# Optimization experiments

Hardware: AMD Instinct MI355X
Metric: run time of the kernel (lower is better)

Reference implementation:

```python
import jax, jax.numpy as jnp
import numpy as np

B, S, D_IN, D_OUT, DEPTH = 4, 2048, 2048, 2048, 11
N_NODES = 2 ** (DEPTH + 1) - 1  # 4095


def setup_inputs() -> dict:
    key = jax.random.key(0)
    k1, k2, k3 = jax.random.split(key, 3)
    x = jax.random.normal(k1, (B, S, D_IN), dtype=jnp.float32)
    # scale weights like Linear init (~1/sqrt(fan_in)) to keep logits sane
    w_in = jax.random.normal(k2, (N_NODES, D_IN), dtype=jnp.float32) * (1.0 / np.sqrt(D_IN))
    w_out = jax.random.normal(k3, (D_OUT, N_NODES), dtype=jnp.float32) * (1.0 / np.sqrt(N_NODES))
    return {"x": x, "w_in": w_in, "w_out": w_out}


def reference(x, w_in, w_out):
    # x: [B,S,D_in]; w_in: [n_nodes, D_in]; w_out: [D_out, n_nodes]
    b, s, _ = x.shape
    cur = jnp.zeros((b, s), dtype=jnp.int32)
    nodes, logits = [], []
    for _ in range(DEPTH + 1):  # fixed, small depth loop (12 iters)
        nodes.append(cur)
        coeffs = w_in[cur]                       # [B,S,D_in] data-dependent gather
        score = jnp.einsum('bsd,bsd->bs', x, coeffs)  # per-token dot product
        logits.append(score)
        cur = cur * 2 + (score >= 0).astype(jnp.int32) + 1
    all_nodes = jnp.stack(nodes, axis=-1)        # [B,S,depth+1]
    all_logits = jnp.stack(logits, axis=-1)      # [B,S,depth+1]
    sel = w_out.T[all_nodes]                     # [B,S,depth+1,D_out]
    mlp1 = jax.nn.gelu(all_logits, approximate=False)  # torch nn.GELU default = exact erf
    return jnp.einsum('bsl,bslw->bsw', mlp1, sel)      # [B,S,D_out]
```

## Files before the change

kernel.cpp:

```cpp
#include <hip/hip_runtime.h>


#define D_IN    2048
#define D_OUT   2048
#define DEPTHP1 12
#define N_NODES 4095
#define N_TOK   8192
#define N_LEAF  2048

__global__ __launch_bounds__(256) void transpose_wout64(
    const float* __restrict__ in, float* __restrict__ out) {
    __shared__ float tile[64][65];
    const int n0 = blockIdx.x * 64;
    const int j0 = blockIdx.y * 64;
    const int tx = threadIdx.x;
    const int ty = threadIdx.y;
    const int n = n0 + tx;
#pragma unroll
    for (int k = 0; k < 16; k++) {
        const int r = ty * 16 + k;
        if (n < N_NODES) tile[r][tx] = in[(size_t)(j0 + r) * N_NODES + n];
    }
    __syncthreads();
#pragma unroll
    for (int k = 0; k < 16; k++) {
        const int r = ty * 16 + k;
        const int nn = n0 + r;
        if (nn < N_NODES) out[(size_t)nn * D_OUT + (j0 + tx)] = tile[tx][r];
    }
}

__global__ __launch_bounds__(256) void phaseA(
    const float* __restrict__ x,
    const float* __restrict__ w_in,
    float* __restrict__ g_all,
    int* __restrict__ leaf,
    int* __restrict__ hist) {
    extern __shared__ float xs[];
    const int wave  = threadIdx.x >> 6;
    const int lane  = threadIdx.x & 63;
    const int token = blockIdx.x * 4 + wave;

    float4* xw = (float4*)(xs) + wave * (D_IN / 4);
    const float4* xrow = (const float4*)(x + (size_t)token * D_IN);
#pragma unroll
    for (int c = 0; c < 8; c++) xw[lane + 64 * c] = xrow[lane + 64 * c];

    int cur = 0;
#pragma unroll
    for (int l = 0; l < DEPTHP1; l++) {
        const float4* wrow = (const float4*)(w_in + (size_t)cur * D_IN);
        float p0 = 0.f, p1 = 0.f, p2 = 0.f, p3 = 0.f;
#pragma unroll
        for (int c = 0; c < 8; c++) {
            const float4 wc = wrow[lane + 64 * c];
            const float4 xc = xw[lane + 64 * c];
            float* p = (c < 2) ? &p0 : (c < 4) ? &p1 : (c < 6) ? &p2 : &p3;
            *p += wc.x * xc.x + wc.y * xc.y + wc.z * xc.z + wc.w * xc.w;
        }
        float part = (p0 + p1) + (p2 + p3);
#pragma unroll
        for (int off = 32; off >= 1; off >>= 1)
            part += __shfl_xor(part, off, 64);
        const float score = part;
        cur = 2 * cur + 1 + (score >= 0.f ? 1 : 0);
        const float g = 0.5f * score * (1.0f + erff(score * 0.70710678118654752f));
        if (lane == 0) g_all[token * DEPTHP1 + l] = g;
    }
    if (lane == 0) {
        const int leafid = ((cur - 1) >> 1) - (N_LEAF - 1);
        leaf[token] = leafid;
        atomicAdd(&hist[leafid], 1);
    }
}

__global__ __launch_bounds__(256) void init_counts(int* __restrict__ p) {
    const int i = blockIdx.x * 256 + threadIdx.x;
    if (i < 2 * N_LEAF) p[i] = 0;
}

__global__ __launch_bounds__(256) void scan2048(
    const int* __restrict__ hist, int* __restrict__ offsets ) {
    __shared__ int vals[N_LEAF];
    __shared__ int partial[256];
    const int t = threadIdx.x;
    int sum = 0;
#pragma unroll
    for (int k = 0; k < 8; k++) {
        const int v = hist[t * 8 + k];
        vals[t * 8 + k] = v;
        sum += v;
    }
    partial[t] = sum;
    __syncthreads();
    for (int off = 1; off < 256; off <<= 1) {
        const int v  = partial[t];
        const int vo = (t >= off) ? partial[t - off] : 0;
        __syncthreads();
        partial[t] = v + vo;
        __syncthreads();
    }
    int base = (t > 0) ? partial[t - 1] : 0;
#pragma unroll
    for (int k = 0; k < 8; k++) {
        offsets[t * 8 + k] = base;
        base += vals[t * 8 + k];
    }
    if (t == 255) offsets[N_LEAF] = base;
}

__global__ __launch_bounds__(256) void scatter_tokens(
    const int* __restrict__ leaf, const int* __restrict__ offsets,
    int* __restrict__ cnt, const float* __restrict__ g_all,
    int* __restrict__ order, float* __restrict__ g_sorted) {
    const int t = blockIdx.x * 256 + threadIdx.x;
    if (t < N_TOK) {
        const int lf = leaf[t];
        const int pos = offsets[lf] + atomicAdd(&cnt[lf], 1);
        order[pos] = t;
#pragma unroll
        for (int l = 0; l < DEPTHP1; l++)
            g_sorted[(size_t)pos * DEPTHP1 + l] = g_all[(size_t)t * DEPTHP1 + l];
    }
}

__global__ __launch_bounds__(256, 2) void phaseB(
    const float* __restrict__ w_out_t,
    const float* __restrict__ g_sorted,
    const int* __restrict__ order,
    const int* __restrict__ offsets,
    float* __restrict__ out) {
    const int lf = ((blockIdx.x & 7) << 8) | (blockIdx.x >> 3);
    const int start = offsets[lf];
    const int end   = offsets[lf + 1];
    if (start == end) return;
    const int t = threadIdx.x;

    int nodes[DEPTHP1];
    const int L = lf + N_LEAF;
#pragma unroll
    for (int l = 0; l < DEPTHP1; l++) nodes[l] = (L >> (DEPTHP1 - 1 - l)) - 1;

    for (int cs = start; cs < end; cs += 8) {
        const int T = end - cs;
        float acc[8][8];
#pragma unroll
        for (int tt = 0; tt < 8; tt++)
#pragma unroll
            for (int k = 0; k < 8; k++) acc[tt][k] = 0.f;

#pragma unroll
        for (int l = 0; l < DEPTHP1; l++) {
            const float4* wr = (const float4*)(w_out_t + (size_t)nodes[l] * D_OUT);
            const float4 w0 = wr[t * 2 + 0];
            const float4 w1 = wr[t * 2 + 1];
#pragma unroll
            for (int tt = 0; tt < 8; tt++) {
                const float g = (tt < T)
                    ? g_sorted[(size_t)(cs + tt) * DEPTHP1 + l] : 0.f;
                acc[tt][0] += g * w0.x; acc[tt][1] += g * w0.y;
                acc[tt][2] += g * w0.z; acc[tt][3] += g * w0.w;
                acc[tt][4] += g * w1.x; acc[tt][5] += g * w1.y;
                acc[tt][6] += g * w1.z; acc[tt][7] += g * w1.w;
            }
        }
#pragma unroll
        for (int tt = 0; tt < 8; tt++) {
            if (tt < T) {
                const int tok = order[cs + tt];
                float4* po = (float4*)(out + (size_t)tok * D_OUT + t * 8);
                float4 o0, o1;
                o0.x = acc[tt][0]; o0.y = acc[tt][1];
                o0.z = acc[tt][2]; o0.w = acc[tt][3];
                o1.x = acc[tt][4]; o1.y = acc[tt][5];
                o1.z = acc[tt][6]; o1.w = acc[tt][7];
                po[0] = o0; po[1] = o1;
            }
        }
    }
}

template <bool TRANSPOSED>
__global__ __launch_bounds__(256) void fff_fused(
    const float* __restrict__ x, const float* __restrict__ w_in,
    const float* __restrict__ w_out, float* __restrict__ out) {
    const int wave  = threadIdx.x >> 6;
    const int lane  = threadIdx.x & 63;
    const int token = blockIdx.x * 4 + wave;
    const float4* xrow = (const float4*)(x + (size_t)token * D_IN);
    float xf[32];
#pragma unroll
    for (int c = 0; c < 8; c++) {
        float4 xc = xrow[lane + 64 * c];
        xf[c * 4 + 0] = xc.x; xf[c * 4 + 1] = xc.y;
        xf[c * 4 + 2] = xc.z; xf[c * 4 + 3] = xc.w;
    }
    float acc[32];
#pragma unroll
    for (int k = 0; k < 32; k++) acc[k] = 0.f;
    int cur = 0;
#pragma unroll
    for (int l = 0; l < DEPTHP1; l++) {
        const float4* wrow = (const float4*)(w_in + (size_t)cur * D_IN);
        float part = 0.f;
#pragma unroll
        for (int c = 0; c < 8; c++) {
            float4 wc = wrow[lane + 64 * c];
            part += wc.x * xf[c * 4 + 0]; part += wc.y * xf[c * 4 + 1];
            part += wc.z * xf[c * 4 + 2]; part += wc.w * xf[c * 4 + 3];
        }
#pragma unroll
        for (int off = 32; off >= 1; off >>= 1) part += __shfl_xor(part, off, 64);
        const float score = part;
        const float g = 0.5f * score * (1.0f + erff(score * 0.70710678118654752f));
        if (TRANSPOSED) {
            const float4* orow = (const float4*)(w_out + (size_t)cur * D_OUT);
#pragma unroll
            for (int c = 0; c < 8; c++) {
                float4 oc = orow[lane + 64 * c];
                acc[c * 4 + 0] += g * oc.x; acc[c * 4 + 1] += g * oc.y;
                acc[c * 4 + 2] += g * oc.z; acc[c * 4 + 3] += g * oc.w;
            }
        } else {
#pragma unroll
            for (int c = 0; c < 8; c++)
#pragma unroll
                for (int k = 0; k < 4; k++) {
                    const int j = (lane + 64 * c) * 4 + k;
                    acc[c * 4 + k] += g * w_out[(size_t)j * N_NODES + cur];
                }
        }
        cur = 2 * cur + 1 + (score >= 0.f ? 1 : 0);
    }
    float4* outrow = (float4*)(out + (size_t)token * D_OUT);
#pragma unroll
    for (int c = 0; c < 8; c++) {
        float4 o;
        o.x = acc[c * 4 + 0]; o.y = acc[c * 4 + 1];
        o.z = acc[c * 4 + 2]; o.w = acc[c * 4 + 3];
        outrow[lane + 64 * c] = o;
    }
}

extern "C" void kernel_launch(void* const* d_in, const int* in_sizes, int n_in,
                              void* d_out, int out_size, void* d_ws, size_t ws_size,
                              hipStream_t stream) {
    (void)in_sizes; (void)n_in; (void)out_size;
    const float* x     = (const float*)d_in[0];
    const float* w_in  = (const float*)d_in[1];
    const float* w_out = (const float*)d_in[2];
    float* out = (float*)d_out;

    const size_t wt_bytes   = (size_t)N_NODES * D_OUT * sizeof(float);
    const size_t g_bytes    = (size_t)N_TOK * DEPTHP1 * sizeof(float);
    const size_t leaf_bytes = (size_t)N_TOK * sizeof(int);
    const size_t ord_bytes  = (size_t)N_TOK * sizeof(int);
    const size_t hist_bytes = (size_t)N_LEAF * sizeof(int);
    const size_t cnt_bytes  = (size_t)N_LEAF * sizeof(int);
    const size_t offs_bytes = (size_t)(N_LEAF + 1) * sizeof(int);
    const size_t gs_bytes   = g_bytes;
    const size_t need = wt_bytes + g_bytes + leaf_bytes + ord_bytes +
                        hist_bytes + cnt_bytes + offs_bytes + gs_bytes + 64;

    if (ws_size >= need) {
        char* p = (char*)d_ws;
        float* w_out_t  = (float*)p;  p += wt_bytes;
        float* g_all    = (float*)p;  p += g_bytes;
        int*   leaf     = (int*)p;    p += leaf_bytes;
        int*   order    = (int*)p;    p += ord_bytes;
        int*   hist     = (int*)p;    p += hist_bytes;
        int*   cnt      = (int*)p;    p += cnt_bytes;
        int*   offsets  = (int*)p;    p += offs_bytes;
        float* g_sorted = (float*)p;

        init_counts<<<(2 * N_LEAF + 255) / 256, 256, 0, stream>>>(hist);
        transpose_wout64<<<dim3((N_NODES + 63) / 64, D_OUT / 64), dim3(64, 4),
                           0, stream>>>(w_out, w_out_t);
        phaseA<<<N_TOK / 4, 256, 4 * D_IN * sizeof(float), stream>>>(
            x, w_in, g_all, leaf, hist);
        scan2048<<<1, 256, 0, stream>>>(hist, offsets);
        scatter_tokens<<<N_TOK / 256, 256, 0, stream>>>(leaf, offsets, cnt,
                                                        g_all, order, g_sorted);
        phaseB<<<N_LEAF, 256, 0, stream>>>(w_out_t, g_sorted, order, offsets, out);
    } else if (ws_size >= wt_bytes) {
        float* w_out_t = (float*)d_ws;
        transpose_wout64<<<dim3((N_NODES + 63) / 64, D_OUT / 64), dim3(64, 4),
                           0, stream>>>(w_out, w_out_t);
        fff_fused<true><<<N_TOK / 4, 256, 0, stream>>>(x, w_in, w_out_t, out);
    } else {
        fff_fused<false><<<N_TOK / 4, 256, 0, stream>>>(x, w_in, w_out, out);
    }
}
```

Baseline: 232.2 us.

## Fuse transpose into routing kernel and replace sort pipeline with per-leaf token scan

Merges the w_out transpose and the tree-routing pass into one launch by interleaving blocks, so the transpose runs alongside routing. The histogram, scan and scatter kernels are removed. Instead, each leaf block of the output phase scans all 8192 leaf ids and collects its own tokens into shared memory with an LDS atomic. This cuts the pipeline from six launches to two and drops the global atomics and sorted copies. In exchange, every one of the 2048 blocks rereads the full leaf array, uses 32KB of LDS, and the token order within a leaf is no longer deterministic.

```diff
diff --git a/kernel.cpp b/kernel.cpp
--- a/kernel.cpp
+++ b/kernel.cpp
@@ -7,6 +7,138 @@
 #define N_NODES 4095
 #define N_TOK   8192
 #define N_LEAF  2048
+
+__global__ __launch_bounds__(256, 4) void fusedA(
+    const float* __restrict__ x,
+    const float* __restrict__ w_in,
+    const float* __restrict__ w_out,
+    float* __restrict__ w_out_t,
+    float* __restrict__ g_all,
+    int* __restrict__ leaf) {
+    extern __shared__ char smem[];
+
+    if (blockIdx.x & 1) {
+        float (*tile)[65] = (float(*)[65])smem;
+        const int tb = blockIdx.x >> 1;
+        const int n0 = (tb & 63) * 64;
+        const int j0 = (tb >> 6) * 64;
+        const int tx = threadIdx.x & 63;
+        const int ty = threadIdx.x >> 6;
+        const int n = n0 + tx;
+#pragma unroll
+        for (int k = 0; k < 16; k++) {
+            const int r = ty * 16 + k;
+            if (n < N_NODES) tile[r][tx] = w_out[(size_t)(j0 + r) * N_NODES + n];
+        }
+        __syncthreads();
+#pragma unroll
+        for (int k = 0; k < 16; k++) {
+            const int r = ty * 16 + k;
+            const int nn = n0 + r;
+            if (nn < N_NODES) w_out_t[(size_t)nn * D_OUT + (j0 + tx)] = tile[tx][r];
+        }
+        return;
+    }
+
+    float* xs = (float*)smem;
+    const int wave  = threadIdx.x >> 6;
+    const int lane  = threadIdx.x & 63;
+    const int token = (blockIdx.x >> 1) * 4 + wave;
+
+    float4* xw = (float4*)xs + wave * (D_IN / 4);
+    const float4* xrow = (const float4*)(x + (size_t)token * D_IN);
+#pragma unroll
+    for (int c = 0; c < 8; c++) xw[lane + 64 * c] = xrow[lane + 64 * c];
+
+    int cur = 0;
+#pragma unroll
+    for (int l = 0; l < DEPTHP1; l++) {
+        const float4* wrow = (const float4*)(w_in + (size_t)cur * D_IN);
+        float4 wv[8];
+#pragma unroll
+        for (int c = 0; c < 8; c++) wv[c] = wrow[lane + 64 * c];
+        float p0 = 0.f, p1 = 0.f, p2 = 0.f, p3 = 0.f;
+#pragma unroll
+        for (int c = 0; c < 8; c++) {
+            const float4 xc = xw[lane + 64 * c];
+            float* p = (c < 2) ? &p0 : (c < 4) ? &p1 : (c < 6) ? &p2 : &p3;
+            *p += wv[c].x * xc.x + wv[c].y * xc.y + wv[c].z * xc.z + wv[c].w * xc.w;
+        }
+        float part = (p0 + p1) + (p2 + p3);
+#pragma unroll
+        for (int off = 32; off >= 1; off >>= 1)
+            part += __shfl_xor(part, off, 64);
+        const float score = part;
+        cur = 2 * cur + 1 + (score >= 0.f ? 1 : 0);
+        const float g = 0.5f * score * (1.0f + erff(score * 0.70710678118654752f));
+        if (lane == 0) g_all[token * DEPTHP1 + l] = g;
+    }
+    if (lane == 0) leaf[token] = ((cur - 1) >> 1) - (N_LEAF - 1);
+}
+
+__global__ __launch_bounds__(256, 2) void phaseB2(
+    const float* __restrict__ w_out_t,
+    const float* __restrict__ g_all,
+    const int* __restrict__ leaf,
+    float* __restrict__ out) {
+    const int lf = ((blockIdx.x & 7) << 8) | (blockIdx.x >> 3);
+    __shared__ int toks[N_TOK];
+    __shared__ int lcount;
+    const int t = threadIdx.x;
+    if (t == 0) lcount = 0;
+    __syncthreads();
+#pragma unroll
+    for (int k = 0; k < N_TOK / 256; k++) {
+        const int tok = k * 256 + t;
+        if (leaf[tok] == lf) toks[atomicAdd(&lcount, 1)] = tok;
+    }
+    __syncthreads();
+    const int n = lcount;
+    if (n == 0) return;
+
+    int nodes[DEPTHP1];
+    const int L = lf + N_LEAF;
+#pragma unroll
+    for (int l = 0; l < DEPTHP1; l++) nodes[l] = (L >> (DEPTHP1 - 1 - l)) - 1;
+
+    for (int cs = 0; cs < n; cs += 8) {
+        const int T = n - cs;
+        float acc[8][8];
+#pragma unroll
+        for (int tt = 0; tt < 8; tt++)
+#pragma unroll
+            for (int k = 0; k < 8; k++) acc[tt][k] = 0.f;
+
+#pragma unroll
+        for (int l = 0; l < DEPTHP1; l++) {
+            const float4* wr = (const float4*)(w_out_t + (size_t)nodes[l] * D_OUT);
+            const float4 w0 = wr[t * 2 + 0];
+            const float4 w1 = wr[t * 2 + 1];
+#pragma unroll
+            for (int tt = 0; tt < 8; tt++) {
+                const float g = (tt < T)
+                    ? g_all[(size_t)toks[cs + tt] * DEPTHP1 + l] : 0.f;
+                acc[tt][0] += g * w0.x; acc[tt][1] += g * w0.y;
+                acc[tt][2] += g * w0.z; acc[tt][3] += g * w0.w;
+                acc[tt][4] += g * w1.x; acc[tt][5] += g * w1.y;
+                acc[tt][6] += g * w1.z; acc[tt][7] += g * w1.w;
+            }
+        }
+#pragma unroll
+        for (int tt = 0; tt < 8; tt++) {
+            if (tt < T) {
+                const int tok = toks[cs + tt];
+                float4* po = (float4*)(out + (size_t)tok * D_OUT + t * 8);
+                float4 o0, o1;
+                o0.x = acc[tt][0]; o0.y = acc[tt][1];
+                o0.z = acc[tt][2]; o0.w = acc[tt][3];
+                o1.x = acc[tt][4]; o1.y = acc[tt][5];
+                o1.z = acc[tt][6]; o1.w = acc[tt][7];
+                po[0] = o0; po[1] = o1;
+            }
+        }
+    }
+}
 
 __global__ __launch_bounds__(256) void transpose_wout64(
     const float* __restrict__ in, float* __restrict__ out) {
@@ -27,156 +159,6 @@
         const int r = ty * 16 + k;
         const int nn = n0 + r;
         if (nn < N_NODES) out[(size_t)nn * D_OUT + (j0 + tx)] = tile[tx][r];
-    }
-}
-
-__global__ __launch_bounds__(256) void phaseA(
-    const float* __restrict__ x,
-    const float* __restrict__ w_in,
-    float* __restrict__ g_all,
-    int* __restrict__ leaf,
-    int* __restrict__ hist) {
-    extern __shared__ float xs[];
-    const int wave  = threadIdx.x >> 6;
-    const int lane  = threadIdx.x & 63;
-    const int token = blockIdx.x * 4 + wave;
-
-    float4* xw = (float4*)(xs) + wave * (D_IN / 4);
-    const float4* xrow = (const float4*)(x + (size_t)token * D_IN);
-#pragma unroll
-    for (int c = 0; c < 8; c++) xw[lane + 64 * c] = xrow[lane + 64 * c];
-
-    int cur = 0;
-#pragma unroll
-    for (int l = 0; l < DEPTHP1; l++) {
-        const float4* wrow = (const float4*)(w_in + (size_t)cur * D_IN);
-        float p0 = 0.f, p1 = 0.f, p2 = 0.f, p3 = 0.f;
-#pragma unroll
-        for (int c = 0; c < 8; c++) {
-            const float4 wc = wrow[lane + 64 * c];
-            const float4 xc = xw[lane + 64 * c];
-            float* p = (c < 2) ? &p0 : (c < 4) ? &p1 : (c < 6) ? &p2 : &p3;
-            *p += wc.x * xc.x + wc.y * xc.y + wc.z * xc.z + wc.w * xc.w;
-        }
-        float part = (p0 + p1) + (p2 + p3);
-#pragma unroll
-        for (int off = 32; off >= 1; off >>= 1)
-            part += __shfl_xor(part, off, 64);
-        const float score = part;
-        cur = 2 * cur + 1 + (score >= 0.f ? 1 : 0);
-        const float g = 0.5f * score * (1.0f + erff(score * 0.70710678118654752f));
-        if (lane == 0) g_all[token * DEPTHP1 + l] = g;
-    }
-    if (lane == 0) {
-        const int leafid = ((cur - 1) >> 1) - (N_LEAF - 1);
-        leaf[token] = leafid;
-        atomicAdd(&hist[leafid], 1);
-    }
-}
-
-__global__ __launch_bounds__(256) void init_counts(int* __restrict__ p) {
-    const int i = blockIdx.x * 256 + threadIdx.x;
-    if (i < 2 * N_LEAF) p[i] = 0;
-}
-
-__global__ __launch_bounds__(256) void scan2048(
-    const int* __restrict__ hist, int* __restrict__ offsets ) {
-    __shared__ int vals[N_LEAF];
-    __shared__ int partial[256];
-    const int t = threadIdx.x;
-    int sum = 0;
-#pragma unroll
-    for (int k = 0; k < 8; k++) {
-        const int v = hist[t * 8 + k];
-        vals[t * 8 + k] = v;
-        sum += v;
-    }
-    partial[t] = sum;
-    __syncthreads();
-    for (int off = 1; off < 256; off <<= 1) {
-        const int v  = partial[t];
-        const int vo = (t >= off) ? partial[t - off] : 0;
-        __syncthreads();
-        partial[t] = v + vo;
-        __syncthreads();
-    }
-    int base = (t > 0) ? partial[t - 1] : 0;
-#pragma unroll
-    for (int k = 0; k < 8; k++) {
-        offsets[t * 8 + k] = base;
-        base += vals[t * 8 + k];
-    }
-    if (t == 255) offsets[N_LEAF] = base;
-}
-
-__global__ __launch_bounds__(256) void scatter_tokens(
-    const int* __restrict__ leaf, const int* __restrict__ offsets,
-    int* __restrict__ cnt, const float* __restrict__ g_all,
-    int* __restrict__ order, float* __restrict__ g_sorted) {
-    const int t = blockIdx.x * 256 + threadIdx.x;
-    if (t < N_TOK) {
-        const int lf = leaf[t];
-        const int pos = offsets[lf] + atomicAdd(&cnt[lf], 1);
-        order[pos] = t;
-#pragma unroll
-        for (int l = 0; l < DEPTHP1; l++)
-            g_sorted[(size_t)pos * DEPTHP1 + l] = g_all[(size_t)t * DEPTHP1 + l];
-    }
-}
-
-__global__ __launch_bounds__(256, 2) void phaseB(
-    const float* __restrict__ w_out_t,
-    const float* __restrict__ g_sorted,
-    const int* __restrict__ order,
-    const int* __restrict__ offsets,
-    float* __restrict__ out) {
-    const int lf = ((blockIdx.x & 7) << 8) | (blockIdx.x >> 3);
-    const int start = offsets[lf];
-    const int end   = offsets[lf + 1];
-    if (start == end) return;
-    const int t = threadIdx.x;
-
-    int nodes[DEPTHP1];
-    const int L = lf + N_LEAF;
-#pragma unroll
-    for (int l = 0; l < DEPTHP1; l++) nodes[l] = (L >> (DEPTHP1 - 1 - l)) - 1;
-
-    for (int cs = start; cs < end; cs += 8) {
-        const int T = end - cs;
-        float acc[8][8];
-#pragma unroll
-        for (int tt = 0; tt < 8; tt++)
-#pragma unroll
-            for (int k = 0; k < 8; k++) acc[tt][k] = 0.f;
-
-#pragma unroll
-        for (int l = 0; l < DEPTHP1; l++) {
-            const float4* wr = (const float4*)(w_out_t + (size_t)nodes[l] * D_OUT);
-            const float4 w0 = wr[t * 2 + 0];
-            const float4 w1 = wr[t * 2 + 1];
-#pragma unroll
-            for (int tt = 0; tt < 8; tt++) {
-                const float g = (tt < T)
-                    ? g_sorted[(size_t)(cs + tt) * DEPTHP1 + l] : 0.f;
-                acc[tt][0] += g * w0.x; acc[tt][1] += g * w0.y;
-                acc[tt][2] += g * w0.z; acc[tt][3] += g * w0.w;
-                acc[tt][4] += g * w1.x; acc[tt][5] += g * w1.y;
-                acc[tt][6] += g * w1.z; acc[tt][7] += g * w1.w;
-            }
-        }
-#pragma unroll
-        for (int tt = 0; tt < 8; tt++) {
-            if (tt < T) {
-                const int tok = order[cs + tt];
-                float4* po = (float4*)(out + (size_t)tok * D_OUT + t * 8);
-                float4 o0, o1;
-                o0.x = acc[tt][0]; o0.y = acc[tt][1];
-                o0.z = acc[tt][2]; o0.w = acc[tt][3];
-                o1.x = acc[tt][4]; o1.y = acc[tt][5];
-                o1.z = acc[tt][6]; o1.w = acc[tt][7];
-                po[0] = o0; po[1] = o1;
-            }
-        }
     }
 }
 
@@ -254,34 +236,17 @@
     const size_t wt_bytes   = (size_t)N_NODES * D_OUT * sizeof(float);
     const size_t g_bytes    = (size_t)N_TOK * DEPTHP1 * sizeof(float);
     const size_t leaf_bytes = (size_t)N_TOK * sizeof(int);
-    const size_t ord_bytes  = (size_t)N_TOK * sizeof(int);
-    const size_t hist_bytes = (size_t)N_LEAF * sizeof(int);
-    const size_t cnt_bytes  = (size_t)N_LEAF * sizeof(int);
-    const size_t offs_bytes = (size_t)(N_LEAF + 1) * sizeof(int);
-    const size_t gs_bytes   = g_bytes;
-    const size_t need = wt_bytes + g_bytes + leaf_bytes + ord_bytes +
-                        hist_bytes + cnt_bytes + offs_bytes + gs_bytes + 64;
+    const size_t need = wt_bytes + g_bytes + leaf_bytes + 64;
 
     if (ws_size >= need) {
         char* p = (char*)d_ws;
-        float* w_out_t  = (float*)p;  p += wt_bytes;
-        float* g_all    = (float*)p;  p += g_bytes;
-        int*   leaf     = (int*)p;    p += leaf_bytes;
-        int*   order    = (int*)p;    p += ord_bytes;
-        int*   hist     = (int*)p;    p += hist_bytes;
-        int*   cnt      = (int*)p;    p += cnt_bytes;
-        int*   offsets  = (int*)p;    p += offs_bytes;
-        float* g_sorted = (float*)p;
-
-        init_counts<<<(2 * N_LEAF + 255) / 256, 256, 0, stream>>>(hist);
-        transpose_wout64<<<dim3((N_NODES + 63) / 64, D_OUT / 64), dim3(64, 4),
-                           0, stream>>>(w_out, w_out_t);
-        phaseA<<<N_TOK / 4, 256, 4 * D_IN * sizeof(float), stream>>>(
-            x, w_in, g_all, leaf, hist);
-        scan2048<<<1, 256, 0, stream>>>(hist, offsets);
-        scatter_tokens<<<N_TOK / 256, 256, 0, stream>>>(leaf, offsets, cnt,
-                                                        g_all, order, g_sorted);
-        phaseB<<<N_LEAF, 256, 0, stream>>>(w_out_t, g_sorted, order, offsets, out);
+        float* w_out_t = (float*)p;  p += wt_bytes;
+        float* g_all   = (float*)p;  p += g_bytes;
+        int*   leaf    = (int*)p;
+
+        fusedA<<<4096, 256, 4 * D_IN * sizeof(float), stream>>>(
+            x, w_in, w_out, w_out_t, g_all, leaf);
+        phaseB2<<<N_LEAF, 256, 0, stream>>>(w_out_t, g_all, leaf, out);
     } else if (ws_size >= wt_bytes) {
         float* w_out_t = (float*)d_ws;
         transpose_wout64<<<dim3((N_NODES + 63) / 64, D_OUT / 64), dim3(64, 4),
```

New measurement: 274.8 us. 1.18x slower.

## Fuse w_out transpose into phase A and cache w_out rows in phase B

Applied to the files above, without the earlier changes.

Merges the w_out transpose and the tree-walk kernel into one launch, with odd blocks doing transpose tiles and even blocks doing routing, so the two memory-bound jobs run side by side. Phase A keeps x in registers instead of shared memory and loads each w_in row before the dot product. GELU moves from phase A into the scatter kernel. Phase B loads the 12 w_out rows once per leaf into registers and stages gate values and token indices in shared memory per chunk, at the cost of more registers and two barriers per chunk.

```diff
diff --git a/kernel.cpp b/kernel.cpp
--- a/kernel.cpp
+++ b/kernel.cpp
@@ -8,55 +8,59 @@
 #define N_TOK   8192
 #define N_LEAF  2048
 
-__global__ __launch_bounds__(256) void transpose_wout64(
-    const float* __restrict__ in, float* __restrict__ out) {
-    __shared__ float tile[64][65];
-    const int n0 = blockIdx.x * 64;
-    const int j0 = blockIdx.y * 64;
-    const int tx = threadIdx.x;
-    const int ty = threadIdx.y;
-    const int n = n0 + tx;
-#pragma unroll
-    for (int k = 0; k < 16; k++) {
-        const int r = ty * 16 + k;
-        if (n < N_NODES) tile[r][tx] = in[(size_t)(j0 + r) * N_NODES + n];
-    }
-    __syncthreads();
-#pragma unroll
-    for (int k = 0; k < 16; k++) {
-        const int r = ty * 16 + k;
-        const int nn = n0 + r;
-        if (nn < N_NODES) out[(size_t)nn * D_OUT + (j0 + tx)] = tile[tx][r];
-    }
-}
-
-__global__ __launch_bounds__(256) void phaseA(
+__global__ __launch_bounds__(256) void fusedA2(
     const float* __restrict__ x,
     const float* __restrict__ w_in,
-    float* __restrict__ g_all,
+    const float* __restrict__ w_out,
+    float* __restrict__ w_out_t,
+    float* __restrict__ s_all,
     int* __restrict__ leaf,
     int* __restrict__ hist) {
-    extern __shared__ float xs[];
+    if (blockIdx.x & 1) {
+        __shared__ float tile[64][65];
+        const int tb = blockIdx.x >> 1;
+        const int n0 = (tb & 63) * 64;
+        const int j0 = (tb >> 6) * 64;
+        const int tx = threadIdx.x & 63;
+        const int ty = threadIdx.x >> 6;
+        const int n = n0 + tx;
+#pragma unroll
+        for (int k = 0; k < 16; k++) {
+            const int r = ty * 16 + k;
+            if (n < N_NODES) tile[r][tx] = w_out[(size_t)(j0 + r) * N_NODES + n];
+        }
+        __syncthreads();
+#pragma unroll
+        for (int k = 0; k < 16; k++) {
+            const int r = ty * 16 + k;
+            const int nn = n0 + r;
+            if (nn < N_NODES) w_out_t[(size_t)nn * D_OUT + (j0 + tx)] = tile[tx][r];
+        }
+        return;
+    }
+
     const int wave  = threadIdx.x >> 6;
     const int lane  = threadIdx.x & 63;
-    const int token = blockIdx.x * 4 + wave;
-
-    float4* xw = (float4*)(xs) + wave * (D_IN / 4);
+    const int token = (blockIdx.x >> 1) * 4 + wave;
+
     const float4* xrow = (const float4*)(x + (size_t)token * D_IN);
-#pragma unroll
-    for (int c = 0; c < 8; c++) xw[lane + 64 * c] = xrow[lane + 64 * c];
+    float4 xf[8];
+#pragma unroll
+    for (int c = 0; c < 8; c++) xf[c] = xrow[lane + 64 * c];
 
     int cur = 0;
 #pragma unroll
     for (int l = 0; l < DEPTHP1; l++) {
         const float4* wrow = (const float4*)(w_in + (size_t)cur * D_IN);
+        float4 wv[8];
+#pragma unroll
+        for (int c = 0; c < 8; c++) wv[c] = wrow[lane + 64 * c];
         float p0 = 0.f, p1 = 0.f, p2 = 0.f, p3 = 0.f;
 #pragma unroll
         for (int c = 0; c < 8; c++) {
-            const float4 wc = wrow[lane + 64 * c];
-            const float4 xc = xw[lane + 64 * c];
             float* p = (c < 2) ? &p0 : (c < 4) ? &p1 : (c < 6) ? &p2 : &p3;
-            *p += wc.x * xc.x + wc.y * xc.y + wc.z * xc.z + wc.w * xc.w;
+            *p += wv[c].x * xf[c].x + wv[c].y * xf[c].y +
+                  wv[c].z * xf[c].z + wv[c].w * xf[c].w;
         }
         float part = (p0 + p1) + (p2 + p3);
 #pragma unroll
@@ -64,8 +68,7 @@
             part += __shfl_xor(part, off, 64);
         const float score = part;
         cur = 2 * cur + 1 + (score >= 0.f ? 1 : 0);
-        const float g = 0.5f * score * (1.0f + erff(score * 0.70710678118654752f));
-        if (lane == 0) g_all[token * DEPTHP1 + l] = g;
+        if (lane == 0) s_all[token * DEPTHP1 + l] = score;
     }
     if (lane == 0) {
         const int leafid = ((cur - 1) >> 1) - (N_LEAF - 1);
@@ -109,9 +112,9 @@
     if (t == 255) offsets[N_LEAF] = base;
 }
 
-__global__ __launch_bounds__(256) void scatter_tokens(
+__global__ __launch_bounds__(256) void scatter_tokens2(
     const int* __restrict__ leaf, const int* __restrict__ offsets,
-    int* __restrict__ cnt, const float* __restrict__ g_all,
+    int* __restrict__ cnt, const float* __restrict__ s_all,
     int* __restrict__ order, float* __restrict__ g_sorted) {
     const int t = blockIdx.x * 256 + threadIdx.x;
     if (t < N_TOK) {
@@ -119,12 +122,15 @@
         const int pos = offsets[lf] + atomicAdd(&cnt[lf], 1);
         order[pos] = t;
 #pragma unroll
-        for (int l = 0; l < DEPTHP1; l++)
-            g_sorted[(size_t)pos * DEPTHP1 + l] = g_all[(size_t)t * DEPTHP1 + l];
-    }
-}
-
-__global__ __launch_bounds__(256, 2) void phaseB(
+        for (int l = 0; l < DEPTHP1; l++) {
+            const float s = s_all[(size_t)t * DEPTHP1 + l];
+            const float g = 0.5f * s * (1.0f + erff(s * 0.70710678118654752f));
+            g_sorted[(size_t)pos * DEPTHP1 + l] = g;
+        }
+    }
+}
+
+__global__ __launch_bounds__(256, 2) void phaseB3(
     const float* __restrict__ w_out_t,
     const float* __restrict__ g_sorted,
     const int* __restrict__ order,
@@ -136,13 +142,31 @@
     if (start == end) return;
     const int t = threadIdx.x;
 
+    __shared__ float gs[96];
+    __shared__ int   ord[8];
+
     int nodes[DEPTHP1];
     const int L = lf + N_LEAF;
 #pragma unroll
     for (int l = 0; l < DEPTHP1; l++) nodes[l] = (L >> (DEPTHP1 - 1 - l)) - 1;
 
+    float4 w0[DEPTHP1], w1[DEPTHP1];
+#pragma unroll
+    for (int l = 0; l < DEPTHP1; l++) {
+        const float4* wr = (const float4*)(w_out_t + (size_t)nodes[l] * D_OUT);
+        w0[l] = wr[t * 2 + 0];
+        w1[l] = wr[t * 2 + 1];
+    }
+
     for (int cs = start; cs < end; cs += 8) {
         const int T = end - cs;
+        __syncthreads();
+        if (t < 96 && (size_t)cs * 12 + t < (size_t)end * 12)
+            gs[t] = g_sorted[(size_t)cs * 12 + t];
+        if (t >= 96 && t < 104 && cs + (t - 96) < end)
+            ord[t - 96] = order[cs + (t - 96)];
+        __syncthreads();
+
         float acc[8][8];
 #pragma unroll
         for (int tt = 0; tt < 8; tt++)
@@ -151,23 +175,19 @@
 
 #pragma unroll
         for (int l = 0; l < DEPTHP1; l++) {
-            const float4* wr = (const float4*)(w_out_t + (size_t)nodes[l] * D_OUT);
-            const float4 w0 = wr[t * 2 + 0];
-            const float4 w1 = wr[t * 2 + 1];
 #pragma unroll
             for (int tt = 0; tt < 8; tt++) {
-                const float g = (tt < T)
-                    ? g_sorted[(size_t)(cs + tt) * DEPTHP1 + l] : 0.f;
-                acc[tt][0] += g * w0.x; acc[tt][1] += g * w0.y;
-                acc[tt][2] += g * w0.z; acc[tt][3] += g * w0.w;
-                acc[tt][4] += g * w1.x; acc[tt][5] += g * w1.y;
-                acc[tt][6] += g * w1.z; acc[tt][7] += g * w1.w;
+                const float g = (tt < T) ? gs[tt * DEPTHP1 + l] : 0.f;
+                acc[tt][0] += g * w0[l].x; acc[tt][1] += g * w0[l].y;
+                acc[tt][2] += g * w0[l].z; acc[tt][3] += g * w0[l].w;
+                acc[tt][4] += g * w1[l].x; acc[tt][5] += g * w1[l].y;
+                acc[tt][6] += g * w1[l].z; acc[tt][7] += g * w1[l].w;
             }
         }
 #pragma unroll
         for (int tt = 0; tt < 8; tt++) {
             if (tt < T) {
-                const int tok = order[cs + tt];
+                const int tok = ord[tt];
                 float4* po = (float4*)(out + (size_t)tok * D_OUT + t * 8);
                 float4 o0, o1;
                 o0.x = acc[tt][0]; o0.y = acc[tt][1];
@@ -177,6 +197,28 @@
                 po[0] = o0; po[1] = o1;
             }
         }
+    }
+}
+
+__global__ __launch_bounds__(256) void transpose_wout64(
+    const float* __restrict__ in, float* __restrict__ out) {
+    __shared__ float tile[64][65];
+    const int n0 = blockIdx.x * 64;
+    const int j0 = blockIdx.y * 64;
+    const int tx = threadIdx.x;
+    const int ty = threadIdx.y;
+    const int n = n0 + tx;
+#pragma unroll
+    for (int k = 0; k < 16; k++) {
+        const int r = ty * 16 + k;
+        if (n < N_NODES) tile[r][tx] = in[(size_t)(j0 + r) * N_NODES + n];
+    }
+    __syncthreads();
+#pragma unroll
+    for (int k = 0; k < 16; k++) {
+        const int r = ty * 16 + k;
+        const int nn = n0 + r;
+        if (nn < N_NODES) out[(size_t)nn * D_OUT + (j0 + tx)] = tile[tx][r];
     }
 }
 
@@ -265,7 +307,7 @@
     if (ws_size >= need) {
         char* p = (char*)d_ws;
         float* w_out_t  = (float*)p;  p += wt_bytes;
-        float* g_all    = (float*)p;  p += g_bytes;
+        float* s_all    = (float*)p;  p += g_bytes;
         int*   leaf     = (int*)p;    p += leaf_bytes;
         int*   order    = (int*)p;    p += ord_bytes;
         int*   hist     = (int*)p;    p += hist_bytes;
@@ -274,14 +316,12 @@
         float* g_sorted = (float*)p;
 
         init_counts<<<(2 * N_LEAF + 255) / 256, 256, 0, stream>>>(hist);
-        transpose_wout64<<<dim3((N_NODES + 63) / 64, D_OUT / 64), dim3(64, 4),
-                           0, stream>>>(w_out, w_out_t);
-        phaseA<<<N_TOK / 4, 256, 4 * D_IN * sizeof(float), stream>>>(
-            x, w_in, g_all, leaf, hist);
+        fusedA2<<<4096, 256, 0, stream>>>(x, w_in, w_out, w_out_t,
+                                          s_all, leaf, hist);
         scan2048<<<1, 256, 0, stream>>>(hist, offsets);
-        scatter_tokens<<<N_TOK / 256, 256, 0, stream>>>(leaf, offsets, cnt,
-                                                        g_all, order, g_sorted);
-        phaseB<<<N_LEAF, 256, 0, stream>>>(w_out_t, g_sorted, order, offsets, out);
+        scatter_tokens2<<<N_TOK / 256, 256, 0, stream>>>(leaf, offsets, cnt,
+                                                         s_all, order, g_sorted);
+        phaseB3<<<N_LEAF, 256, 0, stream>>>(w_out_t, g_sorted, order, offsets, out);
     } else if (ws_size >= wt_bytes) {
         float* w_out_t = (float*)d_ws;
         transpose_wout64<<<dim3((N_NODES + 63) / 64, D_OUT / 64), dim3(64, 4),
```

Measured after the change: 261.2 us. 1.12x slower.

## Split output phase into fixed 32-token ranges with column halves

Applied to the files above, without the earlier changes.

The per-leaf output kernel (one block per leaf, 2048 blocks, many empty or uneven) is replaced by 512 blocks. Each block takes a fixed run of 32 sorted tokens and one half of the output columns. Within its run it walks groups of tokens that share a leaf, loading that leaf's 12 weight rows once per group. A per-position leaf array is written during scatter to find those group boundaries. This aims to balance load across blocks and remove empty blocks, at the cost of reloading weights when a leaf's tokens straddle two ranges and of less weight reuse for large leaves.

```diff
diff --git a/kernel.cpp b/kernel.cpp
--- a/kernel.cpp
+++ b/kernel.cpp
@@ -7,6 +7,8 @@
 #define N_NODES 4095
 #define N_TOK   8192
 #define N_LEAF  2048
+
+typedef float f4 __attribute__((ext_vector_type(4)));
 
 __global__ __launch_bounds__(256) void transpose_wout64(
     const float* __restrict__ in, float* __restrict__ out) {
@@ -112,71 +114,57 @@
 __global__ __launch_bounds__(256) void scatter_tokens(
     const int* __restrict__ leaf, const int* __restrict__ offsets,
     int* __restrict__ cnt, const float* __restrict__ g_all,
-    int* __restrict__ order, float* __restrict__ g_sorted) {
+    int* __restrict__ order, float* __restrict__ g_sorted,
+    int* __restrict__ lf_sorted) {
     const int t = blockIdx.x * 256 + threadIdx.x;
     if (t < N_TOK) {
         const int lf = leaf[t];
         const int pos = offsets[lf] + atomicAdd(&cnt[lf], 1);
         order[pos] = t;
+        lf_sorted[pos] = lf;
 #pragma unroll
         for (int l = 0; l < DEPTHP1; l++)
             g_sorted[(size_t)pos * DEPTHP1 + l] = g_all[(size_t)t * DEPTHP1 + l];
     }
 }
 
-__global__ __launch_bounds__(256, 2) void phaseB(
+__global__ __launch_bounds__(256) void phaseB_cols(
     const float* __restrict__ w_out_t,
     const float* __restrict__ g_sorted,
     const int* __restrict__ order,
-    const int* __restrict__ offsets,
+    const int* __restrict__ lf_sorted,
     float* __restrict__ out) {
-    const int lf = ((blockIdx.x & 7) << 8) | (blockIdx.x >> 3);
-    const int start = offsets[lf];
-    const int end   = offsets[lf + 1];
-    if (start == end) return;
-    const int t = threadIdx.x;
-
-    int nodes[DEPTHP1];
-    const int L = lf + N_LEAF;
-#pragma unroll
-    for (int l = 0; l < DEPTHP1; l++) nodes[l] = (L >> (DEPTHP1 - 1 - l)) - 1;
-
-    for (int cs = start; cs < end; cs += 8) {
-        const int T = end - cs;
-        float acc[8][8];
-#pragma unroll
-        for (int tt = 0; tt < 8; tt++)
-#pragma unroll
-            for (int k = 0; k < 8; k++) acc[tt][k] = 0.f;
-
+    const int b   = blockIdx.x;
+    const int xcd = b & 7;
+    const int j   = b >> 3;
+    const int tr  = xcd * 32 + (j >> 1);
+    const int ct  = j & 1;
+    const int t   = threadIdx.x;
+    const size_t coff = (size_t)ct * 1024 + (size_t)t * 4;
+
+    const int start = tr * 32;
+    const int end   = start + 32;
+
+    int pos = start;
+    while (pos < end) {
+        const int lf = lf_sorted[pos];
+        const int L  = lf + N_LEAF;
+        f4 w[DEPTHP1];
 #pragma unroll
         for (int l = 0; l < DEPTHP1; l++) {
-            const float4* wr = (const float4*)(w_out_t + (size_t)nodes[l] * D_OUT);
-            const float4 w0 = wr[t * 2 + 0];
-            const float4 w1 = wr[t * 2 + 1];
-#pragma unroll
-            for (int tt = 0; tt < 8; tt++) {
-                const float g = (tt < T)
-                    ? g_sorted[(size_t)(cs + tt) * DEPTHP1 + l] : 0.f;
-                acc[tt][0] += g * w0.x; acc[tt][1] += g * w0.y;
-                acc[tt][2] += g * w0.z; acc[tt][3] += g * w0.w;
-                acc[tt][4] += g * w1.x; acc[tt][5] += g * w1.y;
-                acc[tt][6] += g * w1.z; acc[tt][7] += g * w1.w;
-            }
-        }
-#pragma unroll
-        for (int tt = 0; tt < 8; tt++) {
-            if (tt < T) {
-                const int tok = order[cs + tt];
-                float4* po = (float4*)(out + (size_t)tok * D_OUT + t * 8);
-                float4 o0, o1;
-                o0.x = acc[tt][0]; o0.y = acc[tt][1];
-                o0.z = acc[tt][2]; o0.w = acc[tt][3];
-                o1.x = acc[tt][4]; o1.y = acc[tt][5];
-                o1.z = acc[tt][6]; o1.w = acc[tt][7];
-                po[0] = o0; po[1] = o1;
-            }
-        }
+            const int node = (L >> (DEPTHP1 - 1 - l)) - 1;
+            w[l] = *(const f4*)(w_out_t + (size_t)node * D_OUT + coff);
+        }
+        do {
+            const int tok = order[pos];
+            const float* gp = g_sorted + (size_t)pos * DEPTHP1;
+            f4 acc = {0.f, 0.f, 0.f, 0.f};
+#pragma unroll
+            for (int l = 0; l < DEPTHP1; l++)
+                acc += gp[l] * w[l];
+            *(f4*)(out + (size_t)tok * D_OUT + coff) = acc;
+            pos++;
+        } while (pos < end && lf_sorted[pos] == lf);
     }
 }
 
@@ -259,8 +247,10 @@
     const size_t cnt_bytes  = (size_t)N_LEAF * sizeof(int);
     const size_t offs_bytes = (size_t)(N_LEAF + 1) * sizeof(int);
     const size_t gs_bytes   = g_bytes;
+    const size_t lfs_bytes  = (size_t)N_TOK * sizeof(int);
     const size_t need = wt_bytes + g_bytes + leaf_bytes + ord_bytes +
-                        hist_bytes + cnt_bytes + offs_bytes + gs_bytes + 64;
+                        hist_bytes + cnt_bytes + offs_bytes + gs_bytes +
+                        lfs_bytes + 64;
 
     if (ws_size >= need) {
         char* p = (char*)d_ws;
@@ -271,7 +261,8 @@
         int*   hist     = (int*)p;    p += hist_bytes;
         int*   cnt      = (int*)p;    p += cnt_bytes;
         int*   offsets  = (int*)p;    p += offs_bytes;
-        float* g_sorted = (float*)p;
+        float* g_sorted = (float*)p;  p += gs_bytes;
+        int*   lf_sorted= (int*)p;
 
         init_counts<<<(2 * N_LEAF + 255) / 256, 256, 0, stream>>>(hist);
         transpose_wout64<<<dim3((N_NODES + 63) / 64, D_OUT / 64), dim3(64, 4),
@@ -280,8 +271,10 @@
             x, w_in, g_all, leaf, hist);
         scan2048<<<1, 256, 0, stream>>>(hist, offsets);
         scatter_tokens<<<N_TOK / 256, 256, 0, stream>>>(leaf, offsets, cnt,
-                                                        g_all, order, g_sorted);
-        phaseB<<<N_LEAF, 256, 0, stream>>>(w_out_t, g_sorted, order, offsets, out);
+                                                        g_all, order, g_sorted,
+                                                        lf_sorted);
+        phaseB_cols<<<512, 256, 0, stream>>>(w_out_t, g_sorted, order,
+                                             lf_sorted, out);
     } else if (ws_size >= wt_bytes) {
         float* w_out_t = (float*)d_ws;
         transpose_wout64<<<dim3((N_NODES + 63) / 64, D_OUT / 64), dim3(64, 4),
```

After: 240.9 us. 1.04x slower.
